# Performance work log

Measured on AMD Instinct MI355X. Metric: run time of the kernel, lower is better.

The kernel has to match this reference:

```python
import jax, jax.numpy as jnp
import numpy as np

N_NODES = 100000
N_DIH = 1000000
SCALAR_DIM = 128
HIDDEN = 64
ATTR_DIM = 3


def setup_inputs() -> dict:
    key = jax.random.key(0)
    ks = jax.random.split(key, 10)
    x = jax.random.normal(ks[0], (N_NODES, SCALAR_DIM), dtype=jnp.float32)
    quadra_index = jax.random.randint(ks[1], (4, N_DIH), 0, N_NODES, dtype=jnp.int32)
    quadra_attr = jax.random.normal(ks[2], (N_DIH, ATTR_DIM), dtype=jnp.float32)
    d_in = SCALAR_DIM * 2 + ATTR_DIM
    W1 = jax.random.normal(ks[3], (d_in, HIDDEN), dtype=jnp.float32) / np.sqrt(d_in)
    b1 = jnp.zeros((HIDDEN,), dtype=jnp.float32)
    W2 = jax.random.normal(ks[4], (HIDDEN, HIDDEN), dtype=jnp.float32) / np.sqrt(HIDDEN)
    b2 = jnp.zeros((HIDDEN,), dtype=jnp.float32)
    W3 = jax.random.normal(ks[5], (HIDDEN, SCALAR_DIM), dtype=jnp.float32) / np.sqrt(HIDDEN)
    b3 = jnp.zeros((SCALAR_DIM,), dtype=jnp.float32)
    # o3.Linear on pure scalars ('128x0e'->'128x0e') is a bias-free linear map
    Wout = jax.random.normal(ks[6], (SCALAR_DIM, SCALAR_DIM), dtype=jnp.float32) / np.sqrt(SCALAR_DIM)
    return {"x": x, "quadra_index": quadra_index, "quadra_attr": quadra_attr,
            "W1": W1, "b1": b1, "W2": W2, "b2": b2, "W3": W3, "b3": b3, "Wout": Wout}


def _scatter_mean(msgs, idx, num_segments):
    sums = jax.ops.segment_sum(msgs, idx, num_segments=num_segments)
    counts = jax.ops.segment_sum(jnp.ones((msgs.shape[0],), msgs.dtype), idx,
                                 num_segments=num_segments)
    return sums / jnp.maximum(counts, 1.0)[:, None]


def reference(x, quadra_index, quadra_attr, W1, b1, W2, b2, W3, b3, Wout):
    n = x.shape[0]
    x_scalar = x[:, :SCALAR_DIM]
    i, j, k, l = quadra_index[0], quadra_index[1], quadra_index[2], quadra_index[3]
    # gather endpoints, concat with dihedral attrs: [E, 2*D + 3]
    dih_in = jnp.concatenate([x_scalar[i], x_scalar[l], quadra_attr], axis=-1)
    h = jax.nn.silu(dih_in @ W1 + b1)
    h = jax.nn.silu(h @ W2 + b2)
    msgs = h @ W3 + b3  # [E, D]
    aggr_j = _scatter_mean(msgs, j, n)
    aggr_k = _scatter_mean(msgs, k, n)
    aggr = (aggr_j + aggr_k) * 0.5
    return aggr @ Wout
```

## Files before the change

kernel.cpp:

```cpp
#include <hip/hip_runtime.h>

#define N_NODES    100000
#define N_DIH      1000000
#define SCALAR_DIM 128
#define HIDDEN     64
#define ATTR_DIM   3

typedef short v8s __attribute__((ext_vector_type(8)));
typedef float v4f __attribute__((ext_vector_type(4)));
typedef _Float16 v8h __attribute__((ext_vector_type(8)));

__device__ __forceinline__ float silu(float v) {
    return __fdividef(v, 1.0f + __expf(-v));
}

__device__ __forceinline__ unsigned short bf16_rne(float f) {
    unsigned int u = __float_as_uint(f);
    u = (u + 0x7FFFu + ((u >> 16) & 1u)) >> 16;
    return (unsigned short)u;
}

__device__ __forceinline__ float2 bf2_to_f2(unsigned int v) {
    float2 r;
    r.x = __uint_as_float(v << 16);
    r.y = __uint_as_float(v & 0xffff0000u);
    return r;
}

#define PREP_W   112
#define PREP_W34 33
#define PREP_G   64
#define PREP_H   3907
#define PREP_XB  12500
#define PREP_MAIN (PREP_W + PREP_W34 + PREP_G + PREP_H)
#define PREP_ALL  (PREP_MAIN + PREP_XB)

__global__ void prep_kernel(const float* __restrict__ x, unsigned short* __restrict__ xb,
                            const float* __restrict__ W1, const float* __restrict__ W2,
                            const float* __restrict__ W3, const float* __restrict__ b1,
                            const float* __restrict__ b3,
                            const float* __restrict__ Wout,
                            unsigned short* __restrict__ W1f, unsigned short* __restrict__ W2f,
                            unsigned short* __restrict__ W3f, unsigned short* __restrict__ W1g,
                            float* __restrict__ W34, float* __restrict__ b34,
                            float* __restrict__ PK,
                            const int* __restrict__ qidx,
                            int* __restrict__ cnt_j, int* __restrict__ cnt_k,
                            int* __restrict__ rank_j, int* __restrict__ rank_k) {
    const int b = blockIdx.x;
    if (b < PREP_W) {
        const int tid = b * 256 + threadIdx.x;
        if (tid < 16384) {
            const int j = tid & 7, lane = (tid >> 3) & 63, t = tid >> 9;
            const int k = (t >> 2) * 32 + ((lane >> 4) << 3) + j;
            const int n = (t & 3) * 16 + (lane & 15);
            W1f[tid] = bf16_rne(W1[k * 64 + n]);
        } else if (tid < 20480) {
            const int i = tid - 16384;
            const int j = i & 7, lane = (i >> 3) & 63, t = i >> 9;
            const int k = (t >> 2) * 32 + ((lane >> 4) << 3) + j;
            const int n = (t & 3) * 16 + (lane & 15);
            W2f[i] = bf16_rne(W2[k * 64 + n]);
        } else if (tid < 28672) {
            const int i = tid - 20480;
            const int j = i & 7, lane = (i >> 3) & 63, t = i >> 9;
            const int k = (t >> 3) * 32 + ((lane >> 4) << 3) + j;
            const int n = (t & 7) * 16 + (lane & 15);
            W3f[i] = bf16_rne(W3[k * 128 + n]);
        }
    } else if (b < PREP_W + PREP_W34) {
        const int t34 = (b - PREP_W) * 256 + threadIdx.x;
        if (t34 < 8192) {
            const int r = t34 >> 7, c = t34 & 127;
            float s = 0.f;
            #pragma unroll 4
            for (int m = 0; m < 128; ++m) s += W3[r * 128 + m] * Wout[m * 128 + c];
            W34[t34] = s;
        } else if (t34 < 8320) {
            const int c = t34 - 8192;
            float s = 0.f;
            #pragma unroll 4
            for (int m = 0; m < 128; ++m) s += b3[m] * Wout[m * 128 + c];
            b34[c] = s;
        } else if (t34 < 8384) {
            const int c = t34 - 8320;
            PK[c * 4 + 0] = W1[256 * 64 + c];
            PK[c * 4 + 1] = W1[257 * 64 + c];
            PK[c * 4 + 2] = W1[258 * 64 + c];
            PK[c * 4 + 3] = b1[c];
        }
    } else if (b < PREP_W + PREP_W34 + PREP_G) {
        const int i = (b - PREP_W - PREP_W34) * 256 + threadIdx.x;
        const int j = i & 7, lane = (i >> 3) & 63, t = i >> 9;
        const int k = (t >> 3) * 32 + ((lane >> 4) << 3) + j;
        const int n = (t & 7) * 16 + (lane & 15);
        const float w = (n < 64) ? W1[k * 64 + n] : W1[(128 + k) * 64 + (n - 64)];
        W1g[i] = bf16_rne(w);
    } else if (b < PREP_MAIN) {
        const int t = (b - PREP_W - PREP_W34 - PREP_G) * 256 + threadIdx.x;
        if (t < N_DIH) {
            const int rj = atomicAdd(&cnt_j[qidx[N_DIH + t]], 1);
            const int rk = atomicAdd(&cnt_k[qidx[2 * N_DIH + t]], 1);
            if (rank_j != nullptr) {
                rank_j[t] = rj;
                rank_k[t] = rk;
            }
        }
    } else {
        const int t = (b - PREP_MAIN) * 256 + threadIdx.x;
        const float4 v = *(const float4*)&x[(size_t)t * 4];
        ushort4 o;
        o.x = bf16_rne(v.x); o.y = bf16_rne(v.y); o.z = bf16_rne(v.z); o.w = bf16_rne(v.w);
        *(ushort4*)&xb[(size_t)t * 4] = o;
    }
}

__global__ __launch_bounds__(1024) void scan_kernel(const int* __restrict__ cnt_j,
                                                    const int* __restrict__ cnt_k,
                                                    int* __restrict__ off_j, int* __restrict__ off_k) {
    const int* cnt = blockIdx.x ? cnt_k : cnt_j;
    int* off = blockIdx.x ? off_k : off_j;
    __shared__ int wtot[17];
    const int tid = threadIdx.x, lane = tid & 63, wv = tid >> 6;
    int carry = 0;
    for (int base = 0; base < N_NODES; base += 1024) {
        const int i = base + tid;
        const int v = (i < N_NODES) ? cnt[i] : 0;
        int inc = v;
        #pragma unroll
        for (int o = 1; o < 64; o <<= 1) {
            const int t = __shfl_up(inc, o);
            if (lane >= o) inc += t;
        }
        if (lane == 63) wtot[wv] = inc;
        __syncthreads();
        if (tid == 0) {
            int run = 0;
            #pragma unroll
            for (int w = 0; w < 16; ++w) { const int t = wtot[w]; wtot[w] = run; run += t; }
            wtot[16] = run;
        }
        __syncthreads();
        const int excl = inc - v + wtot[wv] + carry;
        if (i < N_NODES) off[i] = excl;
        carry += wtot[16];
        __syncthreads();
    }
    if (tid == 0) off[N_NODES] = carry;
}

__global__ void permute_kernel(const int* __restrict__ qidx,
                               const int* __restrict__ off_j, const int* __restrict__ off_k,
                               const int* __restrict__ rank_j, const int* __restrict__ rank_k,
                               int* __restrict__ perm_j, int* __restrict__ perm_k) {
    const int t = blockIdx.x * blockDim.x + threadIdx.x;
    if (t < N_DIH) {
        const int j = qidx[N_DIH + t];
        perm_j[off_j[j] + rank_j[t]] = t;
        const int k = qidx[2 * N_DIH + t];
        perm_k[off_k[k] + rank_k[t]] = t;
    }
}

#define UVW 3125

__global__ __launch_bounds__(256, 4) void uv_kernel(
    const float* __restrict__ x, const unsigned short* __restrict__ W1g,
    _Float16* __restrict__ uv)
{
    const int tid = threadIdx.x, lane = tid & 63, wv = tid >> 6;
    const int g = blockIdx.x * 4 + wv;
    if (g >= UVW) return;
    const int D0 = g * 32;
    const int m16 = lane & 15, quad = lane >> 4;
    const int r0 = D0 + m16, r1 = D0 + 16 + m16;

    v4f acc[2][8];
    #pragma unroll
    for (int mt = 0; mt < 2; ++mt)
        #pragma unroll
        for (int nt = 0; nt < 8; ++nt) acc[mt][nt] = (v4f){0.f, 0.f, 0.f, 0.f};

    #pragma unroll
    for (int kc = 0; kc < 4; ++kc) {
        const int co = kc * 32 + quad * 8;
        v8s a0, a1;
        {
            const float4 f0 = *(const float4*)&x[(size_t)r0 * 128 + co];
            const float4 f1 = *(const float4*)&x[(size_t)r0 * 128 + co + 4];
            a0[0] = (short)bf16_rne(f0.x); a0[1] = (short)bf16_rne(f0.y);
            a0[2] = (short)bf16_rne(f0.z); a0[3] = (short)bf16_rne(f0.w);
            a0[4] = (short)bf16_rne(f1.x); a0[5] = (short)bf16_rne(f1.y);
            a0[6] = (short)bf16_rne(f1.z); a0[7] = (short)bf16_rne(f1.w);
        }
        {
            const float4 f0 = *(const float4*)&x[(size_t)r1 * 128 + co];
            const float4 f1 = *(const float4*)&x[(size_t)r1 * 128 + co + 4];
            a1[0] = (short)bf16_rne(f0.x); a1[1] = (short)bf16_rne(f0.y);
            a1[2] = (short)bf16_rne(f0.z); a1[3] = (short)bf16_rne(f0.w);
            a1[4] = (short)bf16_rne(f1.x); a1[5] = (short)bf16_rne(f1.y);
            a1[6] = (short)bf16_rne(f1.z); a1[7] = (short)bf16_rne(f1.w);
        }
        #pragma unroll
        for (int nt = 0; nt < 8; ++nt) {
            const v8s bf = *(const v8s*)(W1g + ((kc * 8 + nt) * 64 + lane) * 8);
            acc[0][nt] = __builtin_amdgcn_mfma_f32_16x16x32_bf16(a0, bf, acc[0][nt], 0, 0, 0);
            acc[1][nt] = __builtin_amdgcn_mfma_f32_16x16x32_bf16(a1, bf, acc[1][nt], 0, 0, 0);
        }
    }
    #pragma unroll
    for (int mt = 0; mt < 2; ++mt)
        #pragma unroll
        for (int nt = 0; nt < 8; ++nt) {
            const int c = nt * 16 + m16;
            #pragma unroll
            for (int reg = 0; reg < 4; ++reg) {
                const int n = D0 + mt * 16 + quad * 4 + reg;
                uv[(size_t)n * 128 + c] = (_Float16)acc[mt][nt][reg];
            }
        }
}

#define NW16 62500

__global__ __launch_bounds__(256, 6) void mlp2s_kernel(
    const _Float16* __restrict__ uv, const int* __restrict__ qidx,
    const float* __restrict__ attr, const float* __restrict__ PK,
    const unsigned short* __restrict__ W2f, const float* __restrict__ b2,
    const int* __restrict__ off_j, const int* __restrict__ off_k,
    const int* __restrict__ rank_j, const int* __restrict__ rank_k,
    unsigned short* __restrict__ h2j, unsigned short* __restrict__ h2k)
{
    __shared__ __align__(16) unsigned short hbuf[4][1024];
    const int tid = threadIdx.x, lane = tid & 63, wv = tid >> 6;
    const int g = blockIdx.x * 4 + wv;
    const int D0 = g * 16;
    const int m16 = lane & 15, quad = lane >> 4;
    unsigned short* hs = hbuf[wv];

    const int d = D0 + m16;
    const int irow = qidx[d];
    const int lrow = qidx[3 * N_DIH + d];
    const int jn = qidx[N_DIH + d];
    const int kn = qidx[2 * N_DIH + d];
    const int pj = off_j[jn] + rank_j[d];
    const int pk = off_k[kn] + rank_k[d];

    const _Float16* up = uv + (size_t)irow * 128 + quad * 8;
    const _Float16* vp = uv + (size_t)lrow * 128 + 64 + quad * 8;
    const v8h u0 = *(const v8h*)(up + 0);
    const v8h u1 = *(const v8h*)(up + 32);
    const v8h w0 = *(const v8h*)(vp + 0);
    const v8h w1 = *(const v8h*)(vp + 32);
    const float a0 = attr[(size_t)d * 3 + 0];
    const float a1 = attr[(size_t)d * 3 + 1];
    const float a2 = attr[(size_t)d * 3 + 2];

    const int cb = quad * 8;
    v8s af0, af1;
    #pragma unroll
    for (int e = 0; e < 8; ++e) {
        const float4 pk0 = *(const float4*)&PK[(size_t)(cb + e) * 4];
        const float s0 = (float)u0[e] + (float)w0[e] + pk0.x * a0 + pk0.y * a1 + pk0.z * a2 + pk0.w;
        af0[e] = (short)bf16_rne(silu(s0));
        const float4 pk1 = *(const float4*)&PK[(size_t)(32 + cb + e) * 4];
        const float s1 = (float)u1[e] + (float)w1[e] + pk1.x * a0 + pk1.y * a1 + pk1.z * a2 + pk1.w;
        af1[e] = (short)bf16_rne(silu(s1));
    }

    v4f acc2[4];
    #pragma unroll
    for (int nt = 0; nt < 4; ++nt) acc2[nt] = (v4f){0.f, 0.f, 0.f, 0.f};
    #pragma unroll
    for (int nt = 0; nt < 4; ++nt) {
        const v8s bA = *(const v8s*)(W2f + ((nt) * 64 + lane) * 8);
        const v8s bB = *(const v8s*)(W2f + ((4 + nt) * 64 + lane) * 8);
        acc2[nt] = __builtin_amdgcn_mfma_f32_16x16x32_bf16(af0, bA, acc2[nt], 0, 0, 0);
        acc2[nt] = __builtin_amdgcn_mfma_f32_16x16x32_bf16(af1, bB, acc2[nt], 0, 0, 0);
    }

    #pragma unroll
    for (int nt = 0; nt < 4; ++nt) {
        const int c = nt * 16 + m16;
        const float b2c = b2[c];
        #pragma unroll
        for (int reg = 0; reg < 4; ++reg) {
            const int row = quad * 4 + reg;
            hs[row * 64 + c] = bf16_rne(silu(acc2[nt][reg] + b2c));
        }
    }
    const int sub = lane & 7;
    #pragma unroll
    for (int i = 0; i < 2; ++i) {
        const int row = i * 8 + (lane >> 3);
        const int pjr = __shfl(pj, row);
        const int pkr = __shfl(pk, row);
        const v8s rowv = *(const v8s*)(hs + i * 512 + lane * 8);
        *(v8s*)(h2j + (size_t)pjr * 64 + sub * 8) = rowv;
        *(v8s*)(h2k + (size_t)pkr * 64 + sub * 8) = rowv;
    }
}

__global__ __launch_bounds__(256, 8) void mlp2_kernel(
    const _Float16* __restrict__ uv, const int* __restrict__ qidx,
    const float* __restrict__ attr, const float* __restrict__ PK,
    const unsigned short* __restrict__ W2f, const float* __restrict__ b2,
    unsigned short* __restrict__ h2)
{
    __shared__ __align__(16) unsigned short hbuf[4][1024];
    const int tid = threadIdx.x, lane = tid & 63, wv = tid >> 6;
    const int g = blockIdx.x * 4 + wv;
    const int D0 = g * 16;
    const int m16 = lane & 15, quad = lane >> 4;
    unsigned short* hs = hbuf[wv];

    const int d = D0 + m16;
    const int irow = qidx[d];
    const int lrow = qidx[3 * N_DIH + d];

    const _Float16* up = uv + (size_t)irow * 128 + quad * 8;
    const _Float16* vp = uv + (size_t)lrow * 128 + 64 + quad * 8;
    const v8h u0 = *(const v8h*)(up + 0);
    const v8h u1 = *(const v8h*)(up + 32);
    const v8h w0 = *(const v8h*)(vp + 0);
    const v8h w1 = *(const v8h*)(vp + 32);
    const float a0 = attr[(size_t)d * 3 + 0];
    const float a1 = attr[(size_t)d * 3 + 1];
    const float a2 = attr[(size_t)d * 3 + 2];

    const int cb = quad * 8;
    v8s af0, af1;
    #pragma unroll
    for (int e = 0; e < 8; ++e) {
        const float4 pk0 = *(const float4*)&PK[(size_t)(cb + e) * 4];
        const float s0 = (float)u0[e] + (float)w0[e] + pk0.x * a0 + pk0.y * a1 + pk0.z * a2 + pk0.w;
        af0[e] = (short)bf16_rne(silu(s0));
        const float4 pk1 = *(const float4*)&PK[(size_t)(32 + cb + e) * 4];
        const float s1 = (float)u1[e] + (float)w1[e] + pk1.x * a0 + pk1.y * a1 + pk1.z * a2 + pk1.w;
        af1[e] = (short)bf16_rne(silu(s1));
    }

    v4f acc2[4];
    #pragma unroll
    for (int nt = 0; nt < 4; ++nt) acc2[nt] = (v4f){0.f, 0.f, 0.f, 0.f};
    #pragma unroll
    for (int nt = 0; nt < 4; ++nt) {
        const v8s bA = *(const v8s*)(W2f + ((nt) * 64 + lane) * 8);
        const v8s bB = *(const v8s*)(W2f + ((4 + nt) * 64 + lane) * 8);
        acc2[nt] = __builtin_amdgcn_mfma_f32_16x16x32_bf16(af0, bA, acc2[nt], 0, 0, 0);
        acc2[nt] = __builtin_amdgcn_mfma_f32_16x16x32_bf16(af1, bB, acc2[nt], 0, 0, 0);
    }

    #pragma unroll
    for (int nt = 0; nt < 4; ++nt) {
        const int c = nt * 16 + m16;
        const float b2c = b2[c];
        #pragma unroll
        for (int reg = 0; reg < 4; ++reg) {
            const int row = quad * 4 + reg;
            hs[row * 64 + c] = bf16_rne(silu(acc2[nt][reg] + b2c));
        }
    }
    #pragma unroll
    for (int i = 0; i < 2; ++i) {
        const v8s row16 = *(const v8s*)(hs + i * 512 + lane * 8);
        *(v8s*)(h2 + (size_t)D0 * 64 + i * 512 + lane * 8) = row16;
    }
}

#define NWAVES 31250

__global__ __launch_bounds__(256, 8) void mlp12_kernel(
    const unsigned short* __restrict__ xb, const int* __restrict__ qidx,
    const float* __restrict__ attr,
    const float* __restrict__ W1, const float* __restrict__ b1,
    const float* __restrict__ b2,
    const unsigned short* __restrict__ W1f, const unsigned short* __restrict__ W2f,
    unsigned short* __restrict__ h2)
{
    __shared__ __align__(16) unsigned short hbuf[4][1024];
    const int tid  = threadIdx.x;
    const int lane = tid & 63;
    const int wv   = tid >> 6;
    const int g    = blockIdx.x * 4 + wv;
    const int D0   = g * 16;
    const int m16  = lane & 15;
    const int quad = lane >> 4;
    unsigned short* hs = hbuf[wv];

    const int irow = qidx[D0 + m16];
    const int lrow = qidx[3 * N_DIH + D0 + m16];

    v4f acc[4];
    #pragma unroll
    for (int nt = 0; nt < 4; ++nt) acc[nt] = (v4f){0.f, 0.f, 0.f, 0.f};

    #pragma unroll
    for (int kc = 0; kc < 8; ++kc) {
        const int side = kc >> 2;
        const int coff = (kc & 3) * 32 + quad * 8;
        const int r0 = side ? lrow : irow;
        const v8s a0 = *(const v8s*)(xb + (size_t)r0 * 128 + coff);
        #pragma unroll
        for (int nt = 0; nt < 4; ++nt) {
            const v8s b = *(const v8s*)(W1f + ((kc * 4 + nt) * 64 + lane) * 8);
            acc[nt] = __builtin_amdgcn_mfma_f32_16x16x32_bf16(a0, b, acc[nt], 0, 0, 0);
        }
    }

    #pragma unroll
    for (int nt = 0; nt < 4; ++nt) {
        const int c = nt * 16 + m16;
        const float b1c = b1[c];
        const float wa0 = W1[256 * 64 + c];
        const float wa1 = W1[257 * 64 + c];
        const float wa2 = W1[258 * 64 + c];
        const int quadp = (nt * 2 + (m16 >> 3)) & 3;
        const int jp    = m16 & 7;
        const int kc2   = nt >> 1;
        #pragma unroll
        for (int reg = 0; reg < 4; ++reg) {
            const int r = quad * 4 + reg;
            const int d = D0 + r;
            float v = acc[nt][reg] + b1c
                    + attr[(size_t)d * 3 + 0] * wa0
                    + attr[(size_t)d * 3 + 1] * wa1
                    + attr[(size_t)d * 3 + 2] * wa2;
            v = silu(v);
            hs[kc2 * 512 + (r + 16 * quadp) * 8 + jp] = bf16_rne(v);
        }
    }

    v4f acc2[4];
    #pragma unroll
    for (int nt = 0; nt < 4; ++nt) acc2[nt] = (v4f){0.f, 0.f, 0.f, 0.f};

    #pragma unroll
    for (int kc = 0; kc < 2; ++kc) {
        const v8s a0 = *(const v8s*)(hs + kc * 512 + lane * 8);
        #pragma unroll
        for (int nt = 0; nt < 4; ++nt) {
            const v8s b = *(const v8s*)(W2f + ((kc * 4 + nt) * 64 + lane) * 8);
            acc2[nt] = __builtin_amdgcn_mfma_f32_16x16x32_bf16(a0, b, acc2[nt], 0, 0, 0);
        }
    }

    #pragma unroll
    for (int nt = 0; nt < 4; ++nt) {
        const int c = nt * 16 + m16;
        const float b2c = b2[c];
        #pragma unroll
        for (int reg = 0; reg < 4; ++reg) {
            const int row = quad * 4 + reg;
            hs[row * 64 + c] = bf16_rne(silu(acc2[nt][reg] + b2c));
        }
    }
    #pragma unroll
    for (int i = 0; i < 2; ++i) {
        const v8s row16 = *(const v8s*)(hs + i * 512 + lane * 8);
        *(v8s*)(h2 + (size_t)D0 * 64 + i * 512 + lane * 8) = row16;
    }
}

__global__ __launch_bounds__(256, 2) void aggregate_seq(
    const unsigned short* __restrict__ h2j, const unsigned short* __restrict__ h2k,
    const int* __restrict__ off_j, const int* __restrict__ off_k,
    const float* __restrict__ W34, const float* __restrict__ b34,
    float* __restrict__ out)
{
    __shared__ float a_lds[64 * 132];
    const int tid    = threadIdx.x;
    const int lane   = tid & 63;
    const int wv     = __builtin_amdgcn_readfirstlane(tid >> 6);
    const int base   = blockIdx.x * 64;
    const int half   = lane >> 5;
    const int lane31 = lane & 31;

    for (int p = 0; p < 16; ++p) {
        const int ln = wv * 16 + p;
        const int n  = base + ln;
        float sx = 0.f, sy = 0.f, bf = 0.f;
        if (n < N_NODES) {
            int cj, ck;
            {
                const int e0 = off_j[n], e1 = off_j[n + 1];
                cj = e1 - e0;
                float ax = 0.f, ay = 0.f;
                int e = e0;
                for (; e + 4 <= e1; e += 4) {
                    const float2 fA = bf2_to_f2(*(const unsigned int*)(h2j + (size_t)(e + half) * 64 + lane31 * 2));
                    const float2 fB = bf2_to_f2(*(const unsigned int*)(h2j + (size_t)(e + 2 + half) * 64 + lane31 * 2));
                    ax += fA.x + fB.x; ay += fA.y + fB.y;
                }
                if (e + 2 <= e1) {
                    const float2 f = bf2_to_f2(*(const unsigned int*)(h2j + (size_t)(e + half) * 64 + lane31 * 2));
                    ax += f.x; ay += f.y;
                    e += 2;
                }
                if (e < e1 && half == 0) {
                    const float2 f = bf2_to_f2(*(const unsigned int*)(h2j + (size_t)e * 64 + lane31 * 2));
                    ax += f.x; ay += f.y;
                }
                ax += __shfl_xor(ax, 32);
                ay += __shfl_xor(ay, 32);
                const float inv = 1.0f / (float)max(cj, 1);
                sx += ax * inv; sy += ay * inv;
            }
            {
                const int e0 = off_k[n], e1 = off_k[n + 1];
                ck = e1 - e0;
                float ax = 0.f, ay = 0.f;
                int e = e0;
                for (; e + 4 <= e1; e += 4) {
                    const float2 fA = bf2_to_f2(*(const unsigned int*)(h2k + (size_t)(e + half) * 64 + lane31 * 2));
                    const float2 fB = bf2_to_f2(*(const unsigned int*)(h2k + (size_t)(e + 2 + half) * 64 + lane31 * 2));
                    ax += fA.x + fB.x; ay += fA.y + fB.y;
                }
                if (e + 2 <= e1) {
                    const float2 f = bf2_to_f2(*(const unsigned int*)(h2k + (size_t)(e + half) * 64 + lane31 * 2));
                    ax += f.x; ay += f.y;
                    e += 2;
                }
                if (e < e1 && half == 0) {
                    const float2 f = bf2_to_f2(*(const unsigned int*)(h2k + (size_t)e * 64 + lane31 * 2));
                    ax += f.x; ay += f.y;
                }
                ax += __shfl_xor(ax, 32);
                ay += __shfl_xor(ay, 32);
                const float inv = 1.0f / (float)max(ck, 1);
                sx += ax * inv; sy += ay * inv;
            }
            bf = 0.5f * ((float)(cj > 0) + (float)(ck > 0));
        }
        if (half == 0) {
            float2 w; w.x = sx * 0.5f; w.y = sy * 0.5f;
            *(float2*)&a_lds[ln * 132 + 2 * lane31] = w;
            if (lane31 == 0) a_lds[ln * 132 + 128] = bf;
        }
    }
    __syncthreads();

    const int co = wv * 32;
    const float bfv = a_lds[lane * 132 + 128];
    float acc[32];
    #pragma unroll
    for (int c = 0; c < 32; ++c) acc[c] = bfv * b34[co + c];
    const float* ap = &a_lds[lane * 132];
    #pragma unroll 2
    for (int d = 0; d < 64; d += 4) {
        const float4 av = *(const float4*)&ap[d];
        const float* w0 = &W34[(d + 0) * 128 + co];
        const float* w1 = w0 + 128;
        const float* w2 = w0 + 256;
        const float* w3 = w0 + 384;
        #pragma unroll
        for (int c = 0; c < 32; ++c)
            acc[c] += av.x * w0[c] + av.y * w1[c] + av.z * w2[c] + av.w * w3[c];
    }
    __syncthreads();
    #pragma unroll
    for (int c = 0; c < 32; c += 4)
        *(float4*)&a_lds[lane * 132 + co + c] = make_float4(acc[c], acc[c+1], acc[c+2], acc[c+3]);
    __syncthreads();
    const int q4 = lane31 << 2;
    #pragma unroll
    for (int p = 0; p < 8; ++p) {
        const int ln = wv * 16 + p * 2 + half;
        const int n  = base + ln;
        if (n < N_NODES)
            *(float4*)&out[(size_t)n * 128 + q4] = *(const float4*)&a_lds[ln * 132 + q4];
    }
}

__global__ __launch_bounds__(256, 4) void aggregate_out64(
    const unsigned short* __restrict__ h2,
    const int* __restrict__ off_j, const int* __restrict__ off_k,
    const int* __restrict__ perm_j, const int* __restrict__ perm_k,
    const float* __restrict__ W34, const float* __restrict__ b34,
    float* __restrict__ out)
{
    __shared__ float a_lds[64 * 132];
    const int tid    = threadIdx.x;
    const int lane   = tid & 63;
    const int wv     = __builtin_amdgcn_readfirstlane(tid >> 6);
    const int base   = blockIdx.x * 64;
    const int half   = lane >> 5;
    const int lane31 = lane & 31;

#define AGG_BATCH(B) \
    if (e + B <= e1) { \
        int dd[B]; \
        _Pragma("unroll") \
        for (int q = 0; q < B; ++q) dd[q] = permp[e + q]; \
        unsigned int rr[B]; \
        _Pragma("unroll") \
        for (int q = 0; q < B; ++q) \
            rr[q] = *(const unsigned int*)(h2 + (size_t)dd[q] * 64 + lane31 * 2); \
        _Pragma("unroll") \
        for (int q = 0; q < B; ++q) { \
            const float2 f = bf2_to_f2(rr[q]); \
            ax += f.x; ay += f.y; \
        } \
        e += B; \
    }

    for (int p = 0; p < 8; ++p) {
        const int ln = wv * 16 + p * 2 + half;
        const int n  = base + ln;
        float sx = 0.f, sy = 0.f, bf = 0.f;
        if (n < N_NODES) {
            int cnt2[2];
            #pragma unroll
            for (int li = 0; li < 2; ++li) {
                const int* offp  = li ? off_k  : off_j;
                const int* permp = li ? perm_k : perm_j;
                const int e0 = offp[n], e1 = offp[n + 1];
                cnt2[li] = e1 - e0;
                float ax = 0.f, ay = 0.f;
                int e = e0;
                for (; e + 8 <= e1; ) { AGG_BATCH(8) }
                AGG_BATCH(4)
                AGG_BATCH(2)
                AGG_BATCH(1)
                const float inv = 1.0f / (float)max(cnt2[li], 1);
                sx += ax * inv; sy += ay * inv;
            }
            bf = 0.5f * ((float)(cnt2[0] > 0) + (float)(cnt2[1] > 0));
        }
        float2 w; w.x = sx * 0.5f; w.y = sy * 0.5f;
        *(float2*)&a_lds[ln * 132 + 2 * lane31] = w;
        if (lane31 == 0) a_lds[ln * 132 + 128] = bf;
    }
#undef AGG_BATCH
    __syncthreads();

    const int co = wv * 32;
    const float bfv = a_lds[lane * 132 + 128];
    float acc[32];
    #pragma unroll
    for (int c = 0; c < 32; ++c) acc[c] = bfv * b34[co + c];
    const float* ap = &a_lds[lane * 132];
    #pragma unroll 2
    for (int d = 0; d < 64; d += 4) {
        const float4 av = *(const float4*)&ap[d];
        const float* w0 = &W34[(d + 0) * 128 + co];
        const float* w1 = w0 + 128;
        const float* w2 = w0 + 256;
        const float* w3 = w0 + 384;
        #pragma unroll
        for (int c = 0; c < 32; ++c)
            acc[c] += av.x * w0[c] + av.y * w1[c] + av.z * w2[c] + av.w * w3[c];
    }
    __syncthreads();
    #pragma unroll
    for (int c = 0; c < 32; c += 4)
        *(float4*)&a_lds[lane * 132 + co + c] = make_float4(acc[c], acc[c+1], acc[c+2], acc[c+3]);
    __syncthreads();
    const int q4 = lane31 << 2;
    #pragma unroll
    for (int p = 0; p < 8; ++p) {
        const int ln = wv * 16 + p * 2 + half;
        const int n  = base + ln;
        if (n < N_NODES)
            *(float4*)&out[(size_t)n * 128 + q4] = *(const float4*)&a_lds[ln * 132 + q4];
    }
}

__global__ void scale_kernel(const int* __restrict__ cnt_j, const int* __restrict__ cnt_k,
                             float* __restrict__ scale_j, float* __restrict__ scale_k) {
    int n = blockIdx.x * blockDim.x + threadIdx.x;
    if (n < N_NODES) {
        scale_j[n] = 0.5f / (float)max(cnt_j[n], 1);
        scale_k[n] = 0.5f / (float)max(cnt_k[n], 1);
    }
}

__global__ __launch_bounds__(256, 3) void mlp_mfma_atomic(
    const unsigned short* __restrict__ xb, const int* __restrict__ qidx,
    const float* __restrict__ attr,
    const float* __restrict__ W1, const float* __restrict__ b1,
    const float* __restrict__ b2, const float* __restrict__ b3,
    const unsigned short* __restrict__ W1f, const unsigned short* __restrict__ W2f,
    const unsigned short* __restrict__ W3f,
    const float* __restrict__ scale_j, const float* __restrict__ scale_k,
    float* __restrict__ aggr)
{
    __shared__ __align__(16) unsigned short hbuf[4][4096];
    const int tid  = threadIdx.x;
    const int lane = tid & 63;
    const int wv   = tid >> 6;
    const int g    = blockIdx.x * 4 + wv;
    if (g >= NWAVES) return;
    const int D0   = g * 32;
    const int m16  = lane & 15;
    const int quad = lane >> 4;
    unsigned short* hs = hbuf[wv];

    int irow[2], lrow[2];
    irow[0] = qidx[D0 + m16];
    irow[1] = qidx[D0 + 16 + m16];
    lrow[0] = qidx[3 * N_DIH + D0 + m16];
    lrow[1] = qidx[3 * N_DIH + D0 + 16 + m16];

    v4f acc[2][4];
    #pragma unroll
    for (int mt = 0; mt < 2; ++mt)
        #pragma unroll
        for (int nt = 0; nt < 4; ++nt) acc[mt][nt] = (v4f){0.f, 0.f, 0.f, 0.f};
    #pragma unroll
    for (int kc = 0; kc < 8; ++kc) {
        const int side = kc >> 2;
        const int coff = (kc & 3) * 32 + quad * 8;
        const int r0 = side ? lrow[0] : irow[0];
        const int r1 = side ? lrow[1] : irow[1];
        const v8s a0 = *(const v8s*)(xb + (size_t)r0 * 128 + coff);
        const v8s a1 = *(const v8s*)(xb + (size_t)r1 * 128 + coff);
        #pragma unroll
        for (int nt = 0; nt < 4; ++nt) {
            const v8s b = *(const v8s*)(W1f + ((kc * 4 + nt) * 64 + lane) * 8);
            acc[0][nt] = __builtin_amdgcn_mfma_f32_16x16x32_bf16(a0, b, acc[0][nt], 0, 0, 0);
            acc[1][nt] = __builtin_amdgcn_mfma_f32_16x16x32_bf16(a1, b, acc[1][nt], 0, 0, 0);
        }
    }
    #pragma unroll
    for (int mt = 0; mt < 2; ++mt) {
        #pragma unroll
        for (int nt = 0; nt < 4; ++nt) {
            const int c = nt * 16 + m16;
            const float b1c = b1[c];
            const float wa0 = W1[256 * 64 + c];
            const float wa1 = W1[257 * 64 + c];
            const float wa2 = W1[258 * 64 + c];
            const int quadp = (nt * 2 + (m16 >> 3)) & 3;
            const int jp    = m16 & 7;
            const int kc2   = nt >> 1;
            #pragma unroll
            for (int reg = 0; reg < 4; ++reg) {
                const int r = quad * 4 + reg;
                const int d = D0 + mt * 16 + r;
                float v = acc[mt][nt][reg] + b1c
                        + attr[(size_t)d * 3 + 0] * wa0
                        + attr[(size_t)d * 3 + 1] * wa1
                        + attr[(size_t)d * 3 + 2] * wa2;
                v = silu(v);
                hs[mt * 1024 + kc2 * 512 + (r + 16 * quadp) * 8 + jp] = bf16_rne(v);
            }
        }
    }
    v4f acc2[2][4];
    #pragma unroll
    for (int mt = 0; mt < 2; ++mt)
        #pragma unroll
        for (int nt = 0; nt < 4; ++nt) acc2[mt][nt] = (v4f){0.f, 0.f, 0.f, 0.f};
    #pragma unroll
    for (int kc = 0; kc < 2; ++kc) {
        const v8s a0 = *(const v8s*)(hs +        kc * 512 + lane * 8);
        const v8s a1 = *(const v8s*)(hs + 1024 + kc * 512 + lane * 8);
        #pragma unroll
        for (int nt = 0; nt < 4; ++nt) {
            const v8s b = *(const v8s*)(W2f + ((kc * 4 + nt) * 64 + lane) * 8);
            acc2[0][nt] = __builtin_amdgcn_mfma_f32_16x16x32_bf16(a0, b, acc2[0][nt], 0, 0, 0);
            acc2[1][nt] = __builtin_amdgcn_mfma_f32_16x16x32_bf16(a1, b, acc2[1][nt], 0, 0, 0);
        }
    }
    #pragma unroll
    for (int mt = 0; mt < 2; ++mt) {
        #pragma unroll
        for (int nt = 0; nt < 4; ++nt) {
            const float b2c = b2[nt * 16 + m16];
            const int quadp = (nt * 2 + (m16 >> 3)) & 3;
            const int jp    = m16 & 7;
            const int kc2   = nt >> 1;
            #pragma unroll
            for (int reg = 0; reg < 4; ++reg) {
                const int r = quad * 4 + reg;
                const float v = silu(acc2[mt][nt][reg] + b2c);
                hs[2048 + mt * 1024 + kc2 * 512 + (r + 16 * quadp) * 8 + jp] = bf16_rne(v);
            }
        }
    }
    v4f acc3[2][8];
    #pragma unroll
    for (int mt = 0; mt < 2; ++mt)
        #pragma unroll
        for (int nt = 0; nt < 8; ++nt) acc3[mt][nt] = (v4f){0.f, 0.f, 0.f, 0.f};
    #pragma unroll
    for (int kc = 0; kc < 2; ++kc) {
        const v8s a0 = *(const v8s*)(hs + 2048 +        kc * 512 + lane * 8);
        const v8s a1 = *(const v8s*)(hs + 2048 + 1024 + kc * 512 + lane * 8);
        #pragma unroll
        for (int nt = 0; nt < 8; ++nt) {
            const v8s b = *(const v8s*)(W3f + ((kc * 8 + nt) * 64 + lane) * 8);
            acc3[0][nt] = __builtin_amdgcn_mfma_f32_16x16x32_bf16(a0, b, acc3[0][nt], 0, 0, 0);
            acc3[1][nt] = __builtin_amdgcn_mfma_f32_16x16x32_bf16(a1, b, acc3[1][nt], 0, 0, 0);
        }
    }
    #pragma unroll
    for (int mt = 0; mt < 2; ++mt) {
        int jn[4], kn[4]; float sjv[4], skv[4];
        #pragma unroll
        for (int reg = 0; reg < 4; ++reg) {
            const int d = D0 + mt * 16 + quad * 4 + reg;
            jn[reg] = qidx[N_DIH + d];
            kn[reg] = qidx[2 * N_DIH + d];
            sjv[reg] = scale_j[jn[reg]];
            skv[reg] = scale_k[kn[reg]];
        }
        #pragma unroll
        for (int nt = 0; nt < 8; ++nt) {
            const int c = nt * 16 + m16;
            const float b3c = b3[c];
            #pragma unroll
            for (int reg = 0; reg < 4; ++reg) {
                const float v = acc3[mt][nt][reg] + b3c;
                atomicAdd(&aggr[(size_t)jn[reg] * 128 + c], v * sjv[reg]);
                atomicAdd(&aggr[(size_t)kn[reg] * 128 + c], v * skv[reg]);
            }
        }
    }
}

#define OB    256
#define OTILE 64
__global__ __launch_bounds__(OB, 2) void out_kernel(const float* __restrict__ aggr,
                                                    const float* __restrict__ Wout,
                                                    float* __restrict__ out) {
    __shared__ float a_lds[OTILE * 132];
    const int tid  = threadIdx.x;
    const int lane = tid & 63;
    const int wv   = __builtin_amdgcn_readfirstlane(tid >> 6);
    const int base = blockIdx.x * OTILE;
    const int half = lane >> 5;
    const int q4   = (lane & 31) << 2;
    #pragma unroll
    for (int p = 0; p < 8; ++p) {
        const int ln = wv * 16 + p * 2 + half;
        const int n  = base + ln;
        float4 v = make_float4(0.f, 0.f, 0.f, 0.f);
        if (n < N_NODES) v = *(const float4*)&aggr[(size_t)n * 128 + q4];
        *(float4*)&a_lds[ln * 132 + q4] = v;
    }
    __syncthreads();
    const int c0 = wv * 32;
    float acc[32];
    #pragma unroll
    for (int c = 0; c < 32; ++c) acc[c] = 0.0f;
    const float* ap = &a_lds[lane * 132];
    #pragma unroll 2
    for (int d = 0; d < 128; d += 4) {
        const float4 av = *(const float4*)&ap[d];
        const float* w0 = &Wout[(d + 0) * 128 + c0];
        const float* w1 = &Wout[(d + 1) * 128 + c0];
        const float* w2 = &Wout[(d + 2) * 128 + c0];
        const float* w3 = &Wout[(d + 3) * 128 + c0];
        #pragma unroll
        for (int c = 0; c < 32; ++c)
            acc[c] += av.x * w0[c] + av.y * w1[c] + av.z * w2[c] + av.w * w3[c];
    }
    __syncthreads();
    #pragma unroll
    for (int c = 0; c < 32; c += 4)
        *(float4*)&a_lds[lane * 132 + c0 + c] = make_float4(acc[c], acc[c+1], acc[c+2], acc[c+3]);
    __syncthreads();
    #pragma unroll
    for (int p = 0; p < 8; ++p) {
        const int ln = wv * 16 + p * 2 + half;
        const int n  = base + ln;
        if (n < N_NODES)
            *(float4*)&out[(size_t)n * 128 + q4] = *(const float4*)&a_lds[ln * 132 + q4];
    }
}

extern "C" void kernel_launch(void* const* d_in, const int* in_sizes, int n_in,
                              void* d_out, int out_size, void* d_ws, size_t ws_size,
                              hipStream_t stream) {
    const float* x    = (const float*)d_in[0];
    const int*   qidx = (const int*)d_in[1];
    const float* attr = (const float*)d_in[2];
    const float* W1   = (const float*)d_in[3];
    const float* b1   = (const float*)d_in[4];
    const float* W2   = (const float*)d_in[5];
    const float* b2   = (const float*)d_in[6];
    const float* W3   = (const float*)d_in[7];
    const float* b3   = (const float*)d_in[8];
    const float* Wout = (const float*)d_in[9];
    float* out = (float*)d_out;
    float* wsf = (float*)d_ws;

    const size_t words = ws_size / 4;
    if (words >= (size_t)79300000) {
        size_t o = 0;
        unsigned short* h2j = (unsigned short*)wsf;          o += 32000000;
        unsigned short* h2k = (unsigned short*)(wsf + o);    o += 32000000;
        _Float16* uvp = (_Float16*)(wsf + o);                o += 12800000;
        unsigned short* W1f = (unsigned short*)(wsf + o);    o += 8192;
        unsigned short* W2f = (unsigned short*)(wsf + o);    o += 2048;
        unsigned short* W3f = (unsigned short*)(wsf + o);    o += 4096;
        unsigned short* W1g = (unsigned short*)(wsf + o);    o += 8192;
        float* W34  = wsf + o;                               o += 8192;
        float* b34  = wsf + o;                               o += 128;
        float* PK   = wsf + o;                               o += 256;
        int* cnt_j  = (int*)(wsf + o);                       o += 100000;
        int* cnt_k  = (int*)(wsf + o);                       o += 100000;
        int* off_j  = (int*)(wsf + o);                       o += 100001;
        int* off_k  = (int*)(wsf + o);                       o += 100001;
        int* rank_j = (int*)(wsf + o);                       o += 1000000;
        int* rank_k = (int*)(wsf + o);                       o += 1000000;

        hipMemsetAsync(cnt_j, 0, (size_t)200000 * sizeof(int), stream);
        prep_kernel<<<PREP_MAIN, 256, 0, stream>>>(
            x, h2j , W1, W2, W3, b1, b3, Wout,
            W1f, W2f, W3f, W1g, W34, b34, PK, qidx, cnt_j, cnt_k, rank_j, rank_k);
        scan_kernel<<<2, 1024, 0, stream>>>(cnt_j, cnt_k, off_j, off_k);
        uv_kernel<<<(UVW + 3) / 4, 256, 0, stream>>>(x, W1g, uvp);
        mlp2s_kernel<<<NW16 / 4, 256, 0, stream>>>(
            uvp, qidx, attr, PK, W2f, b2, off_j, off_k, rank_j, rank_k, h2j, h2k);
        aggregate_seq<<<(N_NODES + 63) / 64, 256, 0, stream>>>(
            h2j, h2k, off_j, off_k, W34, b34, out);
    } else if (words >= (size_t)47500000) {
        size_t o = 0;
        unsigned short* h2  = (unsigned short*)wsf;          o += 32000000;
        _Float16* uvp = (_Float16*)(wsf + o);                o += 12800000;
        unsigned short* W1f = (unsigned short*)(wsf + o);    o += 8192;
        unsigned short* W2f = (unsigned short*)(wsf + o);    o += 2048;
        unsigned short* W3f = (unsigned short*)(wsf + o);    o += 4096;
        unsigned short* W1g = (unsigned short*)(wsf + o);    o += 8192;
        float* W34  = wsf + o;                               o += 8192;
        float* b34  = wsf + o;                               o += 128;
        float* PK   = wsf + o;                               o += 256;
        int* cnt_j  = (int*)(wsf + o);                       o += 100000;
        int* cnt_k  = (int*)(wsf + o);                       o += 100000;
        int* off_j  = (int*)(wsf + o);                       o += 100001;
        int* off_k  = (int*)(wsf + o);                       o += 100001;
        int* perm_j = (int*)(wsf + o);                       o += 1000000;
        int* perm_k = (int*)(wsf + o);                       o += 1000000;
        int* rank_j = (int*)h2;
        int* rank_k = rank_j + N_DIH;

        hipMemsetAsync(cnt_j, 0, (size_t)200000 * sizeof(int), stream);
        prep_kernel<<<PREP_MAIN, 256, 0, stream>>>(
            x, h2 , W1, W2, W3, b1, b3, Wout,
            W1f, W2f, W3f, W1g, W34, b34, PK, qidx, cnt_j, cnt_k, rank_j, rank_k);
        scan_kernel<<<2, 1024, 0, stream>>>(cnt_j, cnt_k, off_j, off_k);
        permute_kernel<<<(N_DIH + 255) / 256, 256, 0, stream>>>(
            qidx, off_j, off_k, rank_j, rank_k, perm_j, perm_k);
        uv_kernel<<<(UVW + 3) / 4, 256, 0, stream>>>(x, W1g, uvp);
        mlp2_kernel<<<NW16 / 4, 256, 0, stream>>>(uvp, qidx, attr, PK, W2f, b2, h2);
        aggregate_out64<<<(N_NODES + 63) / 64, 256, 0, stream>>>(
            h2, off_j, off_k, perm_j, perm_k, W34, b34, out);
    } else if (words >= (size_t)41100000) {
        size_t o = 0;
        unsigned short* h2  = (unsigned short*)wsf;          o += 32000000;
        unsigned short* xb  = (unsigned short*)(wsf + o);    o += 6400000;
        unsigned short* W1f = (unsigned short*)(wsf + o);    o += 8192;
        unsigned short* W2f = (unsigned short*)(wsf + o);    o += 2048;
        unsigned short* W3f = (unsigned short*)(wsf + o);    o += 4096;
        float* W34  = wsf + o;                               o += 8192;
        float* b34  = wsf + o;                               o += 128;
        int* cnt_j  = (int*)(wsf + o);                       o += 100000;
        int* cnt_k  = (int*)(wsf + o);                       o += 100000;
        int* off_j  = (int*)(wsf + o);                       o += 100001;
        int* off_k  = (int*)(wsf + o);                       o += 100001;
        int* perm_j = (int*)(wsf + o);                       o += 1000000;
        int* perm_k = (int*)(wsf + o);                       o += 1000000;
        unsigned short* W1g = (unsigned short*)(wsf + o);    o += 8192;
        float* PK   = wsf + o;                               o += 256;
        int* rank_j = (int*)h2;
        int* rank_k = rank_j + N_DIH;

        hipMemsetAsync(cnt_j, 0, (size_t)200000 * sizeof(int), stream);
        prep_kernel<<<PREP_ALL, 256, 0, stream>>>(
            x, xb, W1, W2, W3, b1, b3, Wout,
            W1f, W2f, W3f, W1g, W34, b34, PK, qidx, cnt_j, cnt_k, rank_j, rank_k);
        scan_kernel<<<2, 1024, 0, stream>>>(cnt_j, cnt_k, off_j, off_k);
        permute_kernel<<<(N_DIH + 255) / 256, 256, 0, stream>>>(
            qidx, off_j, off_k, rank_j, rank_k, perm_j, perm_k);
        mlp12_kernel<<<NW16 / 4, 256, 0, stream>>>(
            xb, qidx, attr, W1, b1, b2, W1f, W2f, h2);
        aggregate_out64<<<(N_NODES + 63) / 64, 256, 0, stream>>>(
            h2, off_j, off_k, perm_j, perm_k, W34, b34, out);
    } else {
        int*   cnt_j   = (int*)wsf;
        int*   cnt_k   = cnt_j + N_NODES;
        float* scale_j = wsf + 200000;
        float* scale_k = wsf + 300000;
        float* aggr    = wsf + 400000;
        unsigned short* xb  = (unsigned short*)(wsf + 13200000);
        unsigned short* W1f = (unsigned short*)(wsf + 19600000);
        unsigned short* W2f = (unsigned short*)(wsf + 19608192);
        unsigned short* W3f = (unsigned short*)(wsf + 19610240);
        float* W34 = wsf + 19612288;
        float* b34 = wsf + 19612288;
        unsigned short* W1g = (unsigned short*)(wsf + 19612288);
        float* PK  = wsf + 19612288;

        hipMemsetAsync(cnt_j, 0, (size_t)2 * N_NODES * sizeof(int), stream);
        hipMemsetAsync(aggr, 0, (size_t)N_NODES * 128 * sizeof(float), stream);
        prep_kernel<<<PREP_ALL, 256, 0, stream>>>(
            x, xb, W1, W2, W3, b1, b3, Wout,
            W1f, W2f, W3f, W1g, W34, b34, PK, qidx, cnt_j, cnt_k, nullptr, nullptr);
        scale_kernel<<<(N_NODES + 255) / 256, 256, 0, stream>>>(cnt_j, cnt_k, scale_j, scale_k);
        mlp_mfma_atomic<<<(NWAVES + 3) / 4, 256, 0, stream>>>(
            xb, qidx, attr, W1, b1, b2, b3, W1f, W2f, W3f, scale_j, scale_k, aggr);
        out_kernel<<<(N_NODES + OTILE - 1) / OTILE, OB, 0, stream>>>(aggr, Wout, out);
    }
}
```

Baseline: 538.8 us.

## Shrink aggregate tile to 32 nodes and load perm indices cooperatively via shuffles

The aggregation kernel now handles 32 nodes per block instead of 64 and raises the launch-bounds occupancy hint from 4 to 8. This halves LDS use and the per-thread accumulator array, which should allow more blocks per CU to hide gather latency. Permutation indices are now loaded once per 32-edge chunk, one per lane, and broadcast with shuffles, replacing per-lane redundant scalar loads. In exchange the output projection reloads the W34 rows across twice as many blocks, and the shuffles add extra instructions.

```diff
diff --git a/kernel.cpp b/kernel.cpp
--- a/kernel.cpp
+++ b/kernel.cpp
@@ -572,40 +572,24 @@
     }
 }
 
-__global__ __launch_bounds__(256, 4) void aggregate_out64(
+#define ATILE 32
+__global__ __launch_bounds__(256, 8) void aggregate_out64(
     const unsigned short* __restrict__ h2,
     const int* __restrict__ off_j, const int* __restrict__ off_k,
     const int* __restrict__ perm_j, const int* __restrict__ perm_k,
     const float* __restrict__ W34, const float* __restrict__ b34,
     float* __restrict__ out)
 {
-    __shared__ float a_lds[64 * 132];
+    __shared__ float a_lds[ATILE * 132];
     const int tid    = threadIdx.x;
     const int lane   = tid & 63;
     const int wv     = __builtin_amdgcn_readfirstlane(tid >> 6);
-    const int base   = blockIdx.x * 64;
+    const int base   = blockIdx.x * ATILE;
     const int half   = lane >> 5;
     const int lane31 = lane & 31;
 
-#define AGG_BATCH(B) \
-    if (e + B <= e1) { \
-        int dd[B]; \
-        _Pragma("unroll") \
-        for (int q = 0; q < B; ++q) dd[q] = permp[e + q]; \
-        unsigned int rr[B]; \
-        _Pragma("unroll") \
-        for (int q = 0; q < B; ++q) \
-            rr[q] = *(const unsigned int*)(h2 + (size_t)dd[q] * 64 + lane31 * 2); \
-        _Pragma("unroll") \
-        for (int q = 0; q < B; ++q) { \
-            const float2 f = bf2_to_f2(rr[q]); \
-            ax += f.x; ay += f.y; \
-        } \
-        e += B; \
-    }
-
-    for (int p = 0; p < 8; ++p) {
-        const int ln = wv * 16 + p * 2 + half;
+    for (int p = 0; p < 4; ++p) {
+        const int ln = wv * 8 + p * 2 + half;
         const int n  = base + ln;
         float sx = 0.f, sy = 0.f, bf = 0.f;
         if (n < N_NODES) {
@@ -617,11 +601,30 @@
                 const int e0 = offp[n], e1 = offp[n + 1];
                 cnt2[li] = e1 - e0;
                 float ax = 0.f, ay = 0.f;
-                int e = e0;
-                for (; e + 8 <= e1; ) { AGG_BATCH(8) }
-                AGG_BATCH(4)
-                AGG_BATCH(2)
-                AGG_BATCH(1)
+                for (int eb = e0; eb < e1; eb += 32) {
+                    const int m = min(e1 - eb, 32);
+                    int dv = 0;
+                    if (lane31 < m) dv = permp[eb + lane31];
+                    int q = 0;
+                    for (; q + 8 <= m; q += 8) {
+                        unsigned int rr[8];
+                        #pragma unroll
+                        for (int t = 0; t < 8; ++t) {
+                            const int dq = __shfl(dv, q + t, 32);
+                            rr[t] = *(const unsigned int*)(h2 + (size_t)dq * 64 + lane31 * 2);
+                        }
+                        #pragma unroll
+                        for (int t = 0; t < 8; ++t) {
+                            const float2 f = bf2_to_f2(rr[t]);
+                            ax += f.x; ay += f.y;
+                        }
+                    }
+                    for (; q < m; ++q) {
+                        const int dq = __shfl(dv, q, 32);
+                        const float2 f = bf2_to_f2(*(const unsigned int*)(h2 + (size_t)dq * 64 + lane31 * 2));
+                        ax += f.x; ay += f.y;
+                    }
+                }
                 const float inv = 1.0f / (float)max(cnt2[li], 1);
                 sx += ax * inv; sy += ay * inv;
             }
@@ -631,15 +634,15 @@
         *(float2*)&a_lds[ln * 132 + 2 * lane31] = w;
         if (lane31 == 0) a_lds[ln * 132 + 128] = bf;
     }
-#undef AGG_BATCH
     __syncthreads();
 
-    const int co = wv * 32;
-    const float bfv = a_lds[lane * 132 + 128];
-    float acc[32];
-    #pragma unroll
-    for (int c = 0; c < 32; ++c) acc[c] = bfv * b34[co + c];
-    const float* ap = &a_lds[lane * 132];
+    const int node = lane31;
+    const int co = (wv * 2 + half) * 16;
+    const float bfv = a_lds[node * 132 + 128];
+    float acc[16];
+    #pragma unroll
+    for (int c = 0; c < 16; ++c) acc[c] = bfv * b34[co + c];
+    const float* ap = &a_lds[node * 132];
     #pragma unroll 2
     for (int d = 0; d < 64; d += 4) {
         const float4 av = *(const float4*)&ap[d];
@@ -648,18 +651,18 @@
         const float* w2 = w0 + 256;
         const float* w3 = w0 + 384;
         #pragma unroll
-        for (int c = 0; c < 32; ++c)
+        for (int c = 0; c < 16; ++c)
             acc[c] += av.x * w0[c] + av.y * w1[c] + av.z * w2[c] + av.w * w3[c];
     }
     __syncthreads();
     #pragma unroll
-    for (int c = 0; c < 32; c += 4)
-        *(float4*)&a_lds[lane * 132 + co + c] = make_float4(acc[c], acc[c+1], acc[c+2], acc[c+3]);
+    for (int c = 0; c < 16; c += 4)
+        *(float4*)&a_lds[node * 132 + co + c] = make_float4(acc[c], acc[c+1], acc[c+2], acc[c+3]);
     __syncthreads();
     const int q4 = lane31 << 2;
     #pragma unroll
-    for (int p = 0; p < 8; ++p) {
-        const int ln = wv * 16 + p * 2 + half;
+    for (int p = 0; p < 4; ++p) {
+        const int ln = wv * 8 + p * 2 + half;
         const int n  = base + ln;
         if (n < N_NODES)
             *(float4*)&out[(size_t)n * 128 + q4] = *(const float4*)&a_lds[ln * 132 + q4];
@@ -946,7 +949,7 @@
             qidx, off_j, off_k, rank_j, rank_k, perm_j, perm_k);
         uv_kernel<<<(UVW + 3) / 4, 256, 0, stream>>>(x, W1g, uvp);
         mlp2_kernel<<<NW16 / 4, 256, 0, stream>>>(uvp, qidx, attr, PK, W2f, b2, h2);
-        aggregate_out64<<<(N_NODES + 63) / 64, 256, 0, stream>>>(
+        aggregate_out64<<<(N_NODES + ATILE - 1) / ATILE, 256, 0, stream>>>(
             h2, off_j, off_k, perm_j, perm_k, W34, b34, out);
     } else if (words >= (size_t)41100000) {
         size_t o = 0;
@@ -977,7 +980,7 @@
             qidx, off_j, off_k, rank_j, rank_k, perm_j, perm_k);
         mlp12_kernel<<<NW16 / 4, 256, 0, stream>>>(
             xb, qidx, attr, W1, b1, b2, W1f, W2f, h2);
-        aggregate_out64<<<(N_NODES + 63) / 64, 256, 0, stream>>>(
+        aggregate_out64<<<(N_NODES + ATILE - 1) / ATILE, 256, 0, stream>>>(
             h2, off_j, off_k, perm_j, perm_k, W34, b34, out);
     } else {
         int*   cnt_j   = (int*)wsf;
```

After: 607.1 us. 1.13x slower.
